# Kernel tuning notes

Measured on AMD Instinct MI355X. Metric: run time of the kernel, lower is better.

Reference implementation:

```python
import jax, jax.numpy as jnp
import numpy as np

N_HEAD = 16
D_MODEL = 1024
D_HEAD = D_MODEL // N_HEAD
B, T = 2, 2048


def setup_inputs() -> dict:
    key = jax.random.key(0)
    k1, k2, k3 = jax.random.split(key, 3)
    x = jax.random.normal(k1, (B, T, D_MODEL), dtype=jnp.float32)
    w_attn = jax.random.normal(k2, (3 * D_MODEL, D_MODEL), dtype=jnp.float32) * (D_MODEL ** -0.5)
    w_proj = jax.random.normal(k3, (D_MODEL, D_MODEL), dtype=jnp.float32) * (D_MODEL ** -0.5)
    return {"x": x, "w_attn": w_attn, "w_proj": w_proj}


def _rms_norm(x):
    eps = jnp.asarray(jnp.finfo(x.dtype).eps, x.dtype)
    var = jnp.mean(jnp.square(x), axis=-1, keepdims=True)
    return x * jax.lax.rsqrt(var + eps)


def _rotate_half(x):
    x1, x2 = jnp.split(x, 2, axis=-1)
    return jnp.concatenate((-x2, x1), axis=-1)


def reference(x, w_attn, w_proj):
    Bx, Tx, C = x.shape
    qkv = jnp.einsum('btc,fc->btf', x, w_attn)  # [B,T,3C]
    q, k, v = jnp.split(qkv, 3, axis=-1)
    # [B, H, T, Dh]
    q = q.reshape(Bx, Tx, N_HEAD, D_HEAD).transpose(0, 2, 1, 3)
    k = k.reshape(Bx, Tx, N_HEAD, D_HEAD).transpose(0, 2, 1, 3)
    v = v.reshape(Bx, Tx, N_HEAD, D_HEAD).transpose(0, 2, 1, 3)
    # QK RMSNorm (no learned weight)
    q = _rms_norm(q)
    k = _rms_norm(k)
    # Rotary embedding over full d_head: freqs tiled twice
    inv_freq = 1.0 / (10000.0 ** (jnp.arange(0, D_HEAD, 2, dtype=jnp.float32) / D_HEAD))
    t = jnp.arange(Tx, dtype=jnp.float32)
    freqs = jnp.einsum('i,j->ij', t, inv_freq)  # [T, Dh/2]
    emb = jnp.concatenate((freqs, freqs), axis=-1)  # [T, Dh]
    cos = jnp.cos(emb)[None, None, :, :]
    sin = jnp.sin(emb)[None, None, :, :]
    q = q * cos + _rotate_half(q) * sin
    k = k * cos + _rotate_half(k) * sin
    # Causal SDPA
    scale = D_HEAD ** -0.5
    scores = jnp.einsum('bhqd,bhkd->bhqk', q, k) * scale
    causal = jnp.tril(jnp.ones((Tx, Tx), dtype=bool))
    scores = jnp.where(causal[None, None], scores, jnp.asarray(-jnp.inf, scores.dtype))
    attn = jax.nn.softmax(scores, axis=-1)
    y = jnp.einsum('bhqk,bhkd->bhqd', attn, v)
    y = y.transpose(0, 2, 1, 3).reshape(Bx, Tx, C)
    return jnp.einsum('btc,oc->bto', y, w_proj)
```

## Files before the change

kernel.cpp:

```cpp
#include <hip/hip_runtime.h>
#include <cstdint>
#include <cstddef>


typedef short bf16x8 __attribute__((ext_vector_type(8)));
typedef float floatx4 __attribute__((ext_vector_type(4)));
typedef unsigned short ushortx8 __attribute__((ext_vector_type(8)));
typedef unsigned short ushortx4 __attribute__((ext_vector_type(4)));
typedef unsigned int uintx2 __attribute__((ext_vector_type(2)));

#define DEVI __device__ __forceinline__

DEVI float bf2f(unsigned short u) {
    unsigned int x = ((unsigned int)u) << 16;
    return __builtin_bit_cast(float, x);
}
DEVI unsigned short f2bf(float f) {
    unsigned int u = __builtin_bit_cast(unsigned int, f);
    u += 0x7fffu + ((u >> 16) & 1u);
    return (unsigned short)(u >> 16);
}
DEVI unsigned int pkbf2(float a, float b) {
    unsigned int ua = __builtin_bit_cast(unsigned int, a) + 0x8000u;
    unsigned int ub = __builtin_bit_cast(unsigned int, b) + 0x8000u;
    return __builtin_amdgcn_perm(ub, ua, 0x07060302);
}

DEVI void glds16(const unsigned short* g, unsigned short* l) {
    __builtin_amdgcn_global_load_lds(
        (const __attribute__((address_space(1))) unsigned int*)g,
        (__attribute__((address_space(3))) unsigned int*)l, 16, 0, 0);
}

DEVI void cast8(unsigned short* dst, const float* src) {
    floatx4 a = *(const floatx4*)src;
    floatx4 b = *(const floatx4*)(src + 4);
    ushortx8 o;
    o[0] = f2bf(a[0]); o[1] = f2bf(a[1]); o[2] = f2bf(a[2]); o[3] = f2bf(a[3]);
    o[4] = f2bf(b[0]); o[5] = f2bf(b[1]); o[6] = f2bf(b[2]); o[7] = f2bf(b[3]);
    *(ushortx8*)dst = o;
}

__global__ __launch_bounds__(256)
void cast_inputs(const float* __restrict__ x, const float* __restrict__ wa,
                 const float* __restrict__ wp,
                 unsigned short* __restrict__ xb, unsigned short* __restrict__ wab,
                 unsigned short* __restrict__ wpb)
{
    size_t g = (size_t)blockIdx.x * 256 + threadIdx.x;
    size_t stride = (size_t)gridDim.x * 256;
    for (size_t i = g; i < (4194304 / 8); i += stride) cast8(xb  + i * 8, x  + i * 8);
    for (size_t i = g; i < (3145728 / 8); i += stride) cast8(wab + i * 8, wa + i * 8);
    for (size_t i = g; i < (1048576 / 8); i += stride) cast8(wpb + i * 8, wp + i * 8);
}

template <bool QKV_SPLIT, int BN>
__global__ __launch_bounds__(256)
void gemm_bt(const unsigned short* __restrict__ A, const unsigned short* __restrict__ B,
             unsigned short* __restrict__ Cqk, float* __restrict__ Cf,
             unsigned short* __restrict__ Vt, int M, int N, int K)
{
    constexpr int WCOLS = (BN == 128) ? 2 : 1;
    constexpr int WROWS = 4 / WCOLS;
    constexpr int MI    = 128 / (16 * WROWS);

    __shared__ __align__(16) unsigned short As[128 * 32];
    __shared__ __align__(16) unsigned short Bs[BN * 32];

    const int tid  = threadIdx.x;
    const int lane = tid & 63;
    const int w    = tid >> 6;
    const int wm   = w / WCOLS, wn = w % WCOLS;
    const int quad = lane >> 4;
    const int lm   = lane & 15;
    const int m0 = blockIdx.y * 128;
    const int n0 = blockIdx.x * BN;
    const int sr = lane >> 2;
    const int sc = (lane & 3) * 8;

    floatx4 acc[MI][4] = {};

    for (int k0 = 0; k0 < K; k0 += 32) {
        __syncthreads();
        #pragma unroll
        for (int i = 0; i < 2; ++i) {
            int r = w * 32 + i * 16;
            glds16(&A[(size_t)(m0 + r + sr) * K + k0 + sc], &As[r * 32]);
        }
        #pragma unroll
        for (int i = 0; i < BN / 64; ++i) {
            int r = w * (BN / 4) + i * 16;
            glds16(&B[(size_t)(n0 + r + sr) * K + k0 + sc], &Bs[r * 32]);
        }
        __syncthreads();

        bf16x8 a[MI];
        #pragma unroll
        for (int i = 0; i < MI; ++i)
            a[i] = *(const bf16x8*)&As[(wm * (16 * MI) + i * 16 + lm) * 32 + quad * 8];
        #pragma unroll
        for (int j = 0; j < 4; ++j) {
            bf16x8 b = *(const bf16x8*)&Bs[(wn * 64 + j * 16 + lm) * 32 + quad * 8];
            #pragma unroll
            for (int i = 0; i < MI; ++i)
                acc[i][j] = __builtin_amdgcn_mfma_f32_16x16x32_bf16(a[i], b, acc[i][j], 0, 0, 0);
        }
    }

    #pragma unroll
    for (int i = 0; i < MI; ++i) {
        #pragma unroll
        for (int j = 0; j < 4; ++j) {
            int col = n0 + wn * 64 + j * 16 + lm;
            int row0 = m0 + wm * (16 * MI) + i * 16 + quad * 4;
            if constexpr (QKV_SPLIT) {
                if (col < 2048) {
                    #pragma unroll
                    for (int r = 0; r < 4; ++r)
                        Cqk[(size_t)(row0 + r) * 2048 + col] = f2bf(acc[i][j][r]);
                } else {
                    int bq = row0 >> 11, t0 = row0 & 2047;
                    ushortx4 pk;
                    #pragma unroll
                    for (int r = 0; r < 4; ++r) pk[r] = f2bf(acc[i][j][r]);
                    *(ushortx4*)&Vt[((size_t)(bq * 1024 + (col - 2048))) * 2048 + t0] = pk;
                }
            } else {
                #pragma unroll
                for (int r = 0; r < 4; ++r)
                    Cf[(size_t)(row0 + r) * N + col] = acc[i][j][r];
            }
        }
    }
}

__global__ __launch_bounds__(256)
void rmsnorm_rope(unsigned short* __restrict__ qk)
{
    int gw   = (blockIdx.x * 256 + threadIdx.x) >> 6;
    int lane = threadIdx.x & 63;
    int h = gw & 15;
    int t = (gw >> 4) & 2047;
    int b = gw >> 15;

    size_t base = ((size_t)(b * 2048 + t)) * 2048 + h * 64 + lane;
    float q = bf2f(qk[base]);
    float k = bf2f(qk[base + 1024]);

    float sq = q * q, sk = k * k;
    #pragma unroll
    for (int off = 32; off >= 1; off >>= 1) {
        sq += __shfl_xor(sq, off, 64);
        sk += __shfl_xor(sk, off, 64);
    }
    const float eps = 1.1920929e-07f;
    q *= rsqrtf(sq * (1.0f / 64.0f) + eps);
    k *= rsqrtf(sk * (1.0f / 64.0f) + eps);

    int i = lane & 31;
    float ang = (float)t * expf(-(float)i * 0.28782313662425572f);
    float c = cosf(ang), s = sinf(ang);
    float qp = __shfl_xor(q, 32, 64);
    float kp = __shfl_xor(k, 32, 64);
    float sgn = (lane < 32) ? -1.0f : 1.0f;
    float qo = q * c + sgn * qp * s;
    float ko = k * c + sgn * kp * s;

    qk[base]        = f2bf(qo);
    qk[base + 1024] = f2bf(ko);
}

__global__ __launch_bounds__(256)
void attention(const unsigned short* __restrict__ qk,
               const unsigned short* __restrict__ Vt,
               unsigned short* __restrict__ Y)
{
    constexpr int LD = 72;
    __shared__ __align__(16) unsigned short QPs[64 * LD];
    __shared__ __align__(16) unsigned short Ks [64 * LD];
    __shared__ __align__(16) unsigned short Vs [64 * LD];

    const int tid  = threadIdx.x;
    const int lane = tid & 63;
    const int w    = tid >> 6;
    const int quad = lane >> 4;
    const int lm   = lane & 15;

    const int bh = blockIdx.x;
    const int qt = 31 - blockIdx.y;
    const int b  = bh >> 4, h = bh & 15;
    const int q0 = qt * 64;
    const int qrow = q0 + w * 16 + lm;

    const int r0 = tid >> 3, r1 = r0 + 32, pc = (tid & 7) * 8;
    const unsigned short* kp0 = qk + (size_t)b * 2048 * 2048 + 1024 + h * 64
                              + (size_t)r0 * 2048 + pc;
    const unsigned short* kp1 = kp0 + (size_t)32 * 2048;
    const unsigned short* vp0 = Vt + (size_t)bh * 64 * 2048 + (size_t)r0 * 2048 + pc;
    const unsigned short* vp1 = vp0 + (size_t)32 * 2048;

    #pragma unroll
    for (int i = 0; i < 2; ++i) {
        int c = i * 256 + tid, row = c >> 3, col = (c & 7) * 8;
        *(ushortx8*)&QPs[row * LD + col] =
            *(const ushortx8*)&qk[((size_t)(b * 2048 + q0 + row)) * 2048 + h * 64 + col];
    }

    ushortx8 kreg0 = *(const ushortx8*)kp0, kreg1 = *(const ushortx8*)kp1;
    ushortx8 vreg0 = *(const ushortx8*)vp0, vreg1 = *(const ushortx8*)vp1;
    kp0 += (size_t)64 * 2048; kp1 += (size_t)64 * 2048;
    vp0 += 64; vp1 += 64;

    __syncthreads();
    bf16x8 qf[2];
    #pragma unroll
    for (int kk = 0; kk < 2; ++kk)
        qf[kk] = *(const bf16x8*)&QPs[(w * 16 + lm) * LD + kk * 32 + quad * 8];

    bf16x8 ones;
    #pragma unroll
    for (int i = 0; i < 8; ++i) ones[i] = (short)0x3F80;

    floatx4 o[4] = {};
    floatx4 l_acc = {};
    const float c1 = 0.125f * 1.44269504f;
    const float c2 = 8.0f   * 1.44269504f;

    for (int kt = 0; kt < qt; ++kt) {
        __syncthreads();
        *(ushortx8*)&Ks[r0 * LD + pc] = kreg0;
        *(ushortx8*)&Ks[r1 * LD + pc] = kreg1;
        *(ushortx8*)&Vs[r0 * LD + pc] = vreg0;
        *(ushortx8*)&Vs[r1 * LD + pc] = vreg1;
        __syncthreads();

        kreg0 = *(const ushortx8*)kp0; kreg1 = *(const ushortx8*)kp1;
        vreg0 = *(const ushortx8*)vp0; vreg1 = *(const ushortx8*)vp1;
        kp0 += (size_t)64 * 2048; kp1 += (size_t)64 * 2048;
        vp0 += 64; vp1 += 64;

        floatx4 sa[4] = {};
        #pragma unroll
        for (int kk = 0; kk < 2; ++kk)
            #pragma unroll
            for (int j = 0; j < 4; ++j) {
                bf16x8 kf = *(const bf16x8*)&Ks[(j * 16 + lm) * LD + kk * 32 + quad * 8];
                sa[j] = __builtin_amdgcn_mfma_f32_16x16x32_bf16(kf, qf[kk], sa[j], 0, 0, 0);
            }

        #pragma unroll
        for (int j = 0; j < 4; ++j) {
            float p0 = exp2f(sa[j][0] * c1 - c2);
            float p1 = exp2f(sa[j][1] * c1 - c2);
            float p2 = exp2f(sa[j][2] * c1 - c2);
            float p3 = exp2f(sa[j][3] * c1 - c2);
            uintx2 pk;
            pk[0] = pkbf2(p0, p1);
            pk[1] = pkbf2(p2, p3);
            *(uintx2*)&QPs[(w * 16 + lm) * LD + j * 16 + quad * 4] = pk;
        }

        #pragma unroll
        for (int kk = 0; kk < 2; ++kk) {
            bf16x8 pf = *(const bf16x8*)&QPs[(w * 16 + lm) * LD + kk * 32 + quad * 8];
            #pragma unroll
            for (int j = 0; j < 4; ++j) {
                bf16x8 vf = *(const bf16x8*)&Vs[(j * 16 + lm) * LD + kk * 32 + quad * 8];
                o[j] = __builtin_amdgcn_mfma_f32_16x16x32_bf16(pf, vf, o[j], 0, 0, 0);
            }
            l_acc = __builtin_amdgcn_mfma_f32_16x16x32_bf16(pf, ones, l_acc, 0, 0, 0);
        }
    }

    {
        __syncthreads();
        *(ushortx8*)&Ks[r0 * LD + pc] = kreg0;
        *(ushortx8*)&Ks[r1 * LD + pc] = kreg1;
        *(ushortx8*)&Vs[r0 * LD + pc] = vreg0;
        *(ushortx8*)&Vs[r1 * LD + pc] = vreg1;
        __syncthreads();

        floatx4 sa[4] = {};
        #pragma unroll
        for (int kk = 0; kk < 2; ++kk)
            #pragma unroll
            for (int j = 0; j < 4; ++j) {
                bf16x8 kf = *(const bf16x8*)&Ks[(j * 16 + lm) * LD + kk * 32 + quad * 8];
                sa[j] = __builtin_amdgcn_mfma_f32_16x16x32_bf16(kf, qf[kk], sa[j], 0, 0, 0);
            }

        #pragma unroll
        for (int j = 0; j < 4; ++j) {
            int kb = q0 + j * 16 + quad * 4;
            float p0 = (kb + 0 > qrow) ? 0.0f : exp2f(sa[j][0] * c1 - c2);
            float p1 = (kb + 1 > qrow) ? 0.0f : exp2f(sa[j][1] * c1 - c2);
            float p2 = (kb + 2 > qrow) ? 0.0f : exp2f(sa[j][2] * c1 - c2);
            float p3 = (kb + 3 > qrow) ? 0.0f : exp2f(sa[j][3] * c1 - c2);
            uintx2 pk;
            pk[0] = pkbf2(p0, p1);
            pk[1] = pkbf2(p2, p3);
            *(uintx2*)&QPs[(w * 16 + lm) * LD + j * 16 + quad * 4] = pk;
        }

        #pragma unroll
        for (int kk = 0; kk < 2; ++kk) {
            bf16x8 pf = *(const bf16x8*)&QPs[(w * 16 + lm) * LD + kk * 32 + quad * 8];
            #pragma unroll
            for (int j = 0; j < 4; ++j) {
                bf16x8 vf = *(const bf16x8*)&Vs[(j * 16 + lm) * LD + kk * 32 + quad * 8];
                o[j] = __builtin_amdgcn_mfma_f32_16x16x32_bf16(pf, vf, o[j], 0, 0, 0);
            }
            l_acc = __builtin_amdgcn_mfma_f32_16x16x32_bf16(pf, ones, l_acc, 0, 0, 0);
        }
    }

    float rinv[4];
    #pragma unroll
    for (int r = 0; r < 4; ++r) rinv[r] = 1.0f / l_acc[r];

    #pragma unroll
    for (int j = 0; j < 4; ++j) {
        int colg = h * 64 + j * 16 + lm;
        #pragma unroll
        for (int r = 0; r < 4; ++r) {
            int rowg = q0 + w * 16 + quad * 4 + r;
            Y[((size_t)(b * 2048 + rowg)) * 1024 + colg] = f2bf(o[j][r] * rinv[r]);
        }
    }
}

extern "C" void kernel_launch(void* const* d_in, const int* in_sizes, int n_in,
                              void* d_out, int out_size, void* d_ws, size_t ws_size,
                              hipStream_t stream)
{
    const float* x      = (const float*)d_in[0];
    const float* w_attn = (const float*)d_in[1];
    const float* w_proj = (const float*)d_in[2];
    float* out = (float*)d_out;

    unsigned short* qkbuf = (unsigned short*)d_ws;
    unsigned short* Vtb   = qkbuf + (size_t)4096 * 2048;
    unsigned short* y     = Vtb   + (size_t)32 * 64 * 2048;
    unsigned short* wpb   = y     + (size_t)4096 * 1024;
    unsigned short* xb  = (unsigned short*)d_out;
    unsigned short* wab = xb + (size_t)4096 * 1024;

    dim3 blk(256);
    cast_inputs<<<dim3(1024), blk, 0, stream>>>(x, w_attn, w_proj, xb, wab, wpb);
    gemm_bt<true, 128>
        <<<dim3(24, 32), blk, 0, stream>>>(xb, wab, qkbuf, nullptr, Vtb, 4096, 3072, 1024);
    rmsnorm_rope<<<dim3(16384), blk, 0, stream>>>(qkbuf);
    attention<<<dim3(32, 32), blk, 0, stream>>>(qkbuf, Vtb, y);
    gemm_bt<false, 64>
        <<<dim3(16, 32), blk, 0, stream>>>(y, wpb, nullptr, out, nullptr, 4096, 1024, 1024);
}
```

Measured before the change: 196.0 us.

## Fuse QK RMSNorm and RoPE into QKV GEMM epilogue, parametrize GEMM K-tile

Removes the standalone rmsnorm_rope kernel and applies the per-head RMS normalization and rotary embedding inside the QKV GEMM epilogue, using cross-lane shuffles over the 64 output columns each wave owns. This saves one kernel launch and a full read-modify-write pass over the Q/K buffer. It also adds a BK template parameter and uses a 64-wide K tile for the output projection GEMM, which halves the number of barrier-separated loop iterations there at the cost of more shared memory. The fused epilogue precomputes the rotary frequencies in registers and uses fast __sincosf/__expf instead of the precise versions, which may reduce accuracy at large angles.

```diff
diff --git a/kernel.cpp b/kernel.cpp
--- a/kernel.cpp
+++ b/kernel.cpp
@@ -54,7 +54,7 @@
     for (size_t i = g; i < (1048576 / 8); i += stride) cast8(wpb + i * 8, wp + i * 8);
 }
 
-template <bool QKV_SPLIT, int BN>
+template <bool QKV_SPLIT, int BN, int BK>
 __global__ __launch_bounds__(256)
 void gemm_bt(const unsigned short* __restrict__ A, const unsigned short* __restrict__ B,
              unsigned short* __restrict__ Cqk, float* __restrict__ Cf,
@@ -63,9 +63,11 @@
     constexpr int WCOLS = (BN == 128) ? 2 : 1;
     constexpr int WROWS = 4 / WCOLS;
     constexpr int MI    = 128 / (16 * WROWS);
-
-    __shared__ __align__(16) unsigned short As[128 * 32];
-    __shared__ __align__(16) unsigned short Bs[BN * 32];
+    constexpr int LPR   = BK / 8;
+    constexpr int RPI   = 64 / LPR;
+
+    __shared__ __align__(16) unsigned short As[128 * BK];
+    __shared__ __align__(16) unsigned short Bs[BN * BK];
 
     const int tid  = threadIdx.x;
     const int lane = tid & 63;
@@ -75,99 +77,109 @@
     const int lm   = lane & 15;
     const int m0 = blockIdx.y * 128;
     const int n0 = blockIdx.x * BN;
-    const int sr = lane >> 2;
-    const int sc = (lane & 3) * 8;
+    const int sr = lane / LPR;
+    const int sc = (lane % LPR) * 8;
 
     floatx4 acc[MI][4] = {};
 
-    for (int k0 = 0; k0 < K; k0 += 32) {
-        __syncthreads();
-        #pragma unroll
-        for (int i = 0; i < 2; ++i) {
-            int r = w * 32 + i * 16;
-            glds16(&A[(size_t)(m0 + r + sr) * K + k0 + sc], &As[r * 32]);
-        }
-        #pragma unroll
-        for (int i = 0; i < BN / 64; ++i) {
-            int r = w * (BN / 4) + i * 16;
-            glds16(&B[(size_t)(n0 + r + sr) * K + k0 + sc], &Bs[r * 32]);
-        }
-        __syncthreads();
-
-        bf16x8 a[MI];
-        #pragma unroll
-        for (int i = 0; i < MI; ++i)
-            a[i] = *(const bf16x8*)&As[(wm * (16 * MI) + i * 16 + lm) * 32 + quad * 8];
-        #pragma unroll
-        for (int j = 0; j < 4; ++j) {
-            bf16x8 b = *(const bf16x8*)&Bs[(wn * 64 + j * 16 + lm) * 32 + quad * 8];
+    for (int k0 = 0; k0 < K; k0 += BK) {
+        __syncthreads();
+        #pragma unroll
+        for (int i = 0; i < 32 / RPI; ++i) {
+            int r = w * 32 + i * RPI;
+            glds16(&A[(size_t)(m0 + r + sr) * K + k0 + sc], &As[r * BK]);
+        }
+        #pragma unroll
+        for (int i = 0; i < (BN / 4) / RPI; ++i) {
+            int r = w * (BN / 4) + i * RPI;
+            glds16(&B[(size_t)(n0 + r + sr) * K + k0 + sc], &Bs[r * BK]);
+        }
+        __syncthreads();
+
+        #pragma unroll
+        for (int kk = 0; kk < BK / 32; ++kk) {
+            bf16x8 a[MI];
             #pragma unroll
             for (int i = 0; i < MI; ++i)
-                acc[i][j] = __builtin_amdgcn_mfma_f32_16x16x32_bf16(a[i], b, acc[i][j], 0, 0, 0);
-        }
-    }
-
-    #pragma unroll
-    for (int i = 0; i < MI; ++i) {
-        #pragma unroll
-        for (int j = 0; j < 4; ++j) {
-            int col = n0 + wn * 64 + j * 16 + lm;
-            int row0 = m0 + wm * (16 * MI) + i * 16 + quad * 4;
-            if constexpr (QKV_SPLIT) {
-                if (col < 2048) {
+                a[i] = *(const bf16x8*)&As[(wm * (16 * MI) + i * 16 + lm) * BK + kk * 32 + quad * 8];
+            #pragma unroll
+            for (int j = 0; j < 4; ++j) {
+                bf16x8 b = *(const bf16x8*)&Bs[(wn * 64 + j * 16 + lm) * BK + kk * 32 + quad * 8];
+                #pragma unroll
+                for (int i = 0; i < MI; ++i)
+                    acc[i][j] = __builtin_amdgcn_mfma_f32_16x16x32_bf16(a[i], b, acc[i][j], 0, 0, 0);
+            }
+        }
+    }
+
+    if constexpr (QKV_SPLIT) {
+        const bool is_v = (n0 + wn * 64) >= 2048;
+        if (!is_v) {
+            float rn[MI][4];
+            #pragma unroll
+            for (int i = 0; i < MI; ++i)
+                #pragma unroll
+                for (int r = 0; r < 4; ++r) {
+                    float s = 0.0f;
                     #pragma unroll
-                    for (int r = 0; r < 4; ++r)
-                        Cqk[(size_t)(row0 + r) * 2048 + col] = f2bf(acc[i][j][r]);
-                } else {
+                    for (int j = 0; j < 4; ++j) s += acc[i][j][r] * acc[i][j][r];
+                    s += __shfl_xor(s, 1, 64);
+                    s += __shfl_xor(s, 2, 64);
+                    s += __shfl_xor(s, 4, 64);
+                    s += __shfl_xor(s, 8, 64);
+                    rn[i][r] = rsqrtf(s * (1.0f / 64.0f) + 1.1920929e-07f);
+                }
+            float invf[4];
+            #pragma unroll
+            for (int j = 0; j < 4; ++j) {
+                int d = j * 16 + lm;
+                invf[j] = __expf(-(float)(d & 31) * 0.28782313662425572f);
+            }
+            #pragma unroll
+            for (int i = 0; i < MI; ++i)
+                #pragma unroll
+                for (int r = 0; r < 4; ++r) {
+                    int row = m0 + wm * (16 * MI) + i * 16 + quad * 4 + r;
+                    float t = (float)(row & 2047);
+                    float g = rn[i][r];
+                    #pragma unroll
+                    for (int j = 0; j < 4; ++j) {
+                        int d = j * 16 + lm;
+                        float sn, cs;
+                        __sincosf(t * invf[j], &sn, &cs);
+                        float v  = acc[i][j][r] * g;
+                        float vp = acc[i][j ^ 2][r] * g;
+                        float sgn = (d < 32) ? -1.0f : 1.0f;
+                        Cqk[(size_t)row * 2048 + (n0 + wn * 64 + d)] =
+                            f2bf(v * cs + sgn * vp * sn);
+                    }
+                }
+        } else {
+            #pragma unroll
+            for (int i = 0; i < MI; ++i)
+                #pragma unroll
+                for (int j = 0; j < 4; ++j) {
+                    int col  = n0 + wn * 64 + j * 16 + lm;
+                    int row0 = m0 + wm * (16 * MI) + i * 16 + quad * 4;
                     int bq = row0 >> 11, t0 = row0 & 2047;
                     ushortx4 pk;
                     #pragma unroll
                     for (int r = 0; r < 4; ++r) pk[r] = f2bf(acc[i][j][r]);
                     *(ushortx4*)&Vt[((size_t)(bq * 1024 + (col - 2048))) * 2048 + t0] = pk;
                 }
-            } else {
+        }
+    } else {
+        #pragma unroll
+        for (int i = 0; i < MI; ++i)
+            #pragma unroll
+            for (int j = 0; j < 4; ++j) {
+                int col  = n0 + wn * 64 + j * 16 + lm;
+                int row0 = m0 + wm * (16 * MI) + i * 16 + quad * 4;
                 #pragma unroll
                 for (int r = 0; r < 4; ++r)
                     Cf[(size_t)(row0 + r) * N + col] = acc[i][j][r];
             }
-        }
-    }
-}
-
-__global__ __launch_bounds__(256)
-void rmsnorm_rope(unsigned short* __restrict__ qk)
-{
-    int gw   = (blockIdx.x * 256 + threadIdx.x) >> 6;
-    int lane = threadIdx.x & 63;
-    int h = gw & 15;
-    int t = (gw >> 4) & 2047;
-    int b = gw >> 15;
-
-    size_t base = ((size_t)(b * 2048 + t)) * 2048 + h * 64 + lane;
-    float q = bf2f(qk[base]);
-    float k = bf2f(qk[base + 1024]);
-
-    float sq = q * q, sk = k * k;
-    #pragma unroll
-    for (int off = 32; off >= 1; off >>= 1) {
-        sq += __shfl_xor(sq, off, 64);
-        sk += __shfl_xor(sk, off, 64);
-    }
-    const float eps = 1.1920929e-07f;
-    q *= rsqrtf(sq * (1.0f / 64.0f) + eps);
-    k *= rsqrtf(sk * (1.0f / 64.0f) + eps);
-
-    int i = lane & 31;
-    float ang = (float)t * expf(-(float)i * 0.28782313662425572f);
-    float c = cosf(ang), s = sinf(ang);
-    float qp = __shfl_xor(q, 32, 64);
-    float kp = __shfl_xor(k, 32, 64);
-    float sgn = (lane < 32) ? -1.0f : 1.0f;
-    float qo = q * c + sgn * qp * s;
-    float ko = k * c + sgn * kp * s;
-
-    qk[base]        = f2bf(qo);
-    qk[base + 1024] = f2bf(ko);
+    }
 }
 
 __global__ __launch_bounds__(256)
@@ -347,10 +359,9 @@
 
     dim3 blk(256);
     cast_inputs<<<dim3(1024), blk, 0, stream>>>(x, w_attn, w_proj, xb, wab, wpb);
-    gemm_bt<true, 128>
+    gemm_bt<true, 128, 32>
         <<<dim3(24, 32), blk, 0, stream>>>(xb, wab, qkbuf, nullptr, Vtb, 4096, 3072, 1024);
-    rmsnorm_rope<<<dim3(16384), blk, 0, stream>>>(qkbuf);
     attention<<<dim3(32, 32), blk, 0, stream>>>(qkbuf, Vtb, y);
-    gemm_bt<false, 64>
+    gemm_bt<false, 64, 64>
         <<<dim3(16, 32), blk, 0, stream>>>(y, wpb, nullptr, out, nullptr, 4096, 1024, 1024);
 }
```

After: 184.1 us. 1.06x faster.
